# Performance work log

Hardware: AMD Instinct MI355X
Metric: run time of the kernel (lower is better)

Reference implementation:

```python
import jax, jax.numpy as jnp
import numpy as np

B, N, IN_DIM, SLOT_DIM, NUM_SLOTS, NUM_ITERS = 64, 4096, 256, 256, 8, 3
LN_EPS = 1e-5


def _ln(x, g, b):
    m = jnp.mean(x, axis=-1, keepdims=True)
    v = jnp.mean(jnp.square(x - m), axis=-1, keepdims=True)
    return (x - m) * jax.lax.rsqrt(v + LN_EPS) * g + b


def setup_inputs() -> dict:
    key = jax.random.key(0)
    ks = jax.random.split(key, 16)
    D, I = SLOT_DIM, IN_DIM
    s = 0.02
    return {
        "inputs": jax.random.normal(ks[0], (B, N, I), jnp.float32),
        "slots_noise": jax.random.normal(ks[1], (B, NUM_SLOTS, D), jnp.float32),
        "slots_mu": jax.random.normal(ks[2], (1, 1, D), jnp.float32),
        "slots_log_sigma": jnp.zeros((1, 1, D), jnp.float32),
        "ln_in_g": jnp.ones((I,), jnp.float32), "ln_in_b": jnp.zeros((I,), jnp.float32),
        "ln_s_g": jnp.ones((D,), jnp.float32), "ln_s_b": jnp.zeros((D,), jnp.float32),
        "ln_m_g": jnp.ones((D,), jnp.float32), "ln_m_b": jnp.zeros((D,), jnp.float32),
        "Wq": jax.random.normal(ks[3], (D, D), jnp.float32) * s,
        "Wk": jax.random.normal(ks[4], (I, D), jnp.float32) * s,
        "Wv": jax.random.normal(ks[5], (I, D), jnp.float32) * s,
        "gru_w_ih": jax.random.normal(ks[6], (3 * D, D), jnp.float32) * s,
        "gru_w_hh": jax.random.normal(ks[7], (3 * D, D), jnp.float32) * s,
        "gru_b_ih": jnp.zeros((3 * D,), jnp.float32),
        "gru_b_hh": jnp.zeros((3 * D,), jnp.float32),
        "mlp_w1": jax.random.normal(ks[8], (D, 4 * D), jnp.float32) * s,
        "mlp_b1": jnp.zeros((4 * D,), jnp.float32),
        "mlp_w2": jax.random.normal(ks[9], (4 * D, D), jnp.float32) * s,
        "mlp_b2": jnp.zeros((D,), jnp.float32),
    }


def reference(inputs, slots_noise, slots_mu, slots_log_sigma, ln_in_g, ln_in_b,
              ln_s_g, ln_s_b, ln_m_g, ln_m_b, Wq, Wk, Wv,
              gru_w_ih, gru_w_hh, gru_b_ih, gru_b_hh,
              mlp_w1, mlp_b1, mlp_w2, mlp_b2):
    D = SLOT_DIM
    # slot init: mu + sigma * noise
    slots = slots_mu + jnp.exp(slots_log_sigma) * slots_noise  # [B, S, D]
    x = _ln(inputs, ln_in_g, ln_in_b)                          # [B, N, I]
    k = x @ Wk                                                 # [B, N, D]
    v = x @ Wv                                                 # [B, N, D]
    scale = 1.0 / jnp.sqrt(jnp.float32(D))
    attn = None
    for _ in range(NUM_ITERS):
        slots_prev = slots
        s_n = _ln(slots, ln_s_g, ln_s_b)
        q = s_n @ Wq                                           # [B, S, D]
        logits = jnp.einsum('bnd,bmd->bnm', k, q) * scale      # [B, N, S]
        attn = jax.nn.softmax(logits, axis=-1)                 # softmax over slots
        attn_nrm = attn / (jnp.sum(attn, axis=1, keepdims=True) + 1e-8)
        updates = jnp.einsum('bnm,bnd->bmd', attn_nrm, v)      # [B, S, D]
        # GRUCell (PyTorch semantics)
        gi = updates @ gru_w_ih.T + gru_b_ih                   # [B, S, 3D]
        gh = slots_prev @ gru_w_hh.T + gru_b_hh
        gi_r, gi_z, gi_n = jnp.split(gi, 3, axis=-1)
        gh_r, gh_z, gh_n = jnp.split(gh, 3, axis=-1)
        r = jax.nn.sigmoid(gi_r + gh_r)
        z = jax.nn.sigmoid(gi_z + gh_z)
        n = jnp.tanh(gi_n + r * gh_n)
        slots = (1.0 - z) * n + z * slots_prev
        # residual MLP
        h = jax.nn.relu(_ln(slots, ln_m_g, ln_m_b) @ mlp_w1 + mlp_b1)
        slots = slots + h @ mlp_w2 + mlp_b2
    return slots, jnp.transpose(attn, (0, 2, 1))
```

## Files before the change

### kernel.cpp

```cpp
#include <hip/hip_runtime.h>


typedef unsigned short u16;
typedef __attribute__((ext_vector_type(8))) short bf16x8;
typedef __attribute__((ext_vector_type(4))) float f32x4;

#define MFMA16(a, b, c) __builtin_amdgcn_mfma_f32_16x16x32_bf16((a), (b), (c), 0, 0, 0)

__device__ __forceinline__ u16 f2bf(float f) {
  union { float f; unsigned u; } v; v.f = f;
  unsigned r = (v.u + 0x7fffu + ((v.u >> 16) & 1u)) >> 16;
  return (u16)r;
}
__device__ __forceinline__ float sigm(float x) { return 1.f / (1.f + __expf(-x)); }
__device__ __forceinline__ float tanh_f(float x) { return 1.f - 2.f / (1.f + __expf(2.f * x)); }

__global__ __launch_bounds__(256) void prep_kernel(
    const float* __restrict__ Wq, const float* __restrict__ Wk, const float* __restrict__ Wv,
    const float* __restrict__ wih, const float* __restrict__ whh,
    const float* __restrict__ w1, const float* __restrict__ w2,
    u16* __restrict__ wkB, u16* __restrict__ wqT, u16* __restrict__ wvT,
    u16* __restrict__ wihB, u16* __restrict__ whhB, u16* __restrict__ w1T, u16* __restrict__ w2T) {
  int gid = blockIdx.x * 256 + threadIdx.x;
  int stride = gridDim.x * 256;
  for (int i = gid; i < 65536; i += stride) wkB[i] = f2bf(Wk[i]);
  for (int i = gid; i < 65536; i += stride) { int d = i >> 8, e = i & 255; wqT[i] = f2bf(Wq[e * 256 + d]); }
  for (int i = gid; i < 65536; i += stride) { int d = i >> 8, ii = i & 255; wvT[i] = f2bf(Wv[ii * 256 + d]); }
  for (int i = gid; i < 196608; i += stride) wihB[i] = f2bf(wih[i]);
  for (int i = gid; i < 196608; i += stride) whhB[i] = f2bf(whh[i]);
  for (int i = gid; i < 262144; i += stride) { int j = i >> 8, e = i & 255; w1T[i] = f2bf(w1[e * 1024 + j]); }
  for (int i = gid; i < 262144; i += stride) { int d = i >> 10, j = i & 1023; w2T[i] = f2bf(w2[j * 256 + d]); }
}

__device__ __forceinline__ void ln_row16(const float (*src)[264], u16 (*dst)[264],
                                         const float* __restrict__ g, const float* __restrict__ bb,
                                         int wave, int lane) {
  int row = wave;
  if (row < 8) {
    float4 v = *reinterpret_cast<const float4*>(&src[row][lane * 4]);
    float s = v.x + v.y + v.z + v.w;
    float sq = v.x * v.x + v.y * v.y + v.z * v.z + v.w * v.w;
#pragma unroll
    for (int m = 1; m < 64; m <<= 1) { s += __shfl_xor(s, m); sq += __shfl_xor(sq, m); }
    float mu = s * (1.f / 256.f);
    float var = sq * (1.f / 256.f) - mu * mu;
    float rstd = rsqrtf(fmaxf(var, 0.f) + 1e-5f);
    float4 gg = *reinterpret_cast<const float4*>(&g[lane * 4]);
    float4 bv = *reinterpret_cast<const float4*>(&bb[lane * 4]);
    unsigned lo = (unsigned)f2bf((v.x - mu) * rstd * gg.x + bv.x) |
                  ((unsigned)f2bf((v.y - mu) * rstd * gg.y + bv.y) << 16);
    unsigned hi = (unsigned)f2bf((v.z - mu) * rstd * gg.z + bv.z) |
                  ((unsigned)f2bf((v.w - mu) * rstd * gg.w + bv.w) << 16);
    *reinterpret_cast<uint2*>(&dst[row][lane * 4]) = make_uint2(lo, hi);
  } else if (row < 16) {
    *reinterpret_cast<uint2*>(&dst[row][lane * 4]) = make_uint2(0, 0);
  }
}

__global__ __launch_bounds__(1024, 4) void slot_kernel(
    float* __restrict__ slots, u16* __restrict__ qg, float* __restrict__ cd,
    const float* __restrict__ wsY, const float* __restrict__ wsS,
    const u16* __restrict__ wvT, const u16* __restrict__ wihB, const u16* __restrict__ whhB,
    const u16* __restrict__ w1T, const u16* __restrict__ w2T, const u16* __restrict__ wqT,
    const u16* __restrict__ wkB,
    const float* __restrict__ bih, const float* __restrict__ bhh,
    const float* __restrict__ b1v, const float* __restrict__ b2v,
    const float* __restrict__ g_in, const float* __restrict__ b_in,
    const float* __restrict__ g_s, const float* __restrict__ b_s,
    const float* __restrict__ g_m, const float* __restrict__ b_m,
    const float* __restrict__ s_mu, const float* __restrict__ s_ls,
    const float* __restrict__ noise,
    float* __restrict__ d_out, int do_update) {
  __shared__ alignas(16) char pool[58368];
  u16 (*h_lds)[1032] = reinterpret_cast<u16(*)[1032]>(pool);
  u16 (*u_lds)[264] = reinterpret_cast<u16(*)[264]>(pool);
  u16 (*uv_lds)[264] = reinterpret_cast<u16(*)[264]>(pool + 8448);
  u16 (*sb_lds)[264] = reinterpret_cast<u16(*)[264]>(pool + 16896);
  u16 (*m_lds)[264] = reinterpret_cast<u16(*)[264]>(pool + 33024);
  float (*ns_lds)[264] = reinterpret_cast<float(*)[264]>(pool + 41472);
  u16 (*q_lds)[264] = reinterpret_cast<u16(*)[264]>(pool + 41472);
  __shared__ float sS0[16], sS1[16], sInv[16];
  __shared__ float redq[16][4][4][2];

  const int b = blockIdx.x;
  const int tid = threadIdx.x;
  const int lane = tid & 63, wave = tid >> 6;
  const int quad = lane >> 4, col = lane & 15;
  const int i256 = tid & 255, s4 = tid >> 8;
  const f32x4 vzero = {0.f, 0.f, 0.f, 0.f};

  if (do_update) {
    if (tid < 16) {
      float S0 = 0.f, S1 = 0.f;
      if (tid < 8) {
        for (int c = 0; c < 8; c++) {
          S0 += wsS[((b * 8 + c) * 8 + tid) * 2 + 0];
          S1 += wsS[((b * 8 + c) * 8 + tid) * 2 + 1];
        }
      }
      sS0[tid] = S0; sS1[tid] = S1; sInv[tid] = 1.f / (S0 + 1e-8f);
    }
#pragma unroll
    for (int r = 0; r < 4; r++) {
      int s = s4 + r * 4;
      sb_lds[s][i256] = (s < 8) ? f2bf(slots[(size_t)(b * 8 + s) * 256 + i256]) : (u16)0;
    }
    __syncthreads();
    {
      float gv = g_in[i256], bv = b_in[i256];
#pragma unroll
      for (int r = 0; r < 4; r++) {
        int s = s4 + r * 4;
        if (s < 8) {
          float y = 0.f;
#pragma unroll
          for (int c = 0; c < 8; c++) y += wsY[((size_t)((b * 8 + c) * 8 + s)) * 256 + i256];
          u_lds[s][i256] = f2bf((gv * (y - sS1[s]) + bv * sS0[s]) * sInv[s]);
        } else {
          u_lds[s][i256] = 0;
        }
      }
    }
    __syncthreads();
    {
      bf16x8 af[8];
#pragma unroll
      for (int k = 0; k < 8; k++)
        af[k] = *reinterpret_cast<const bf16x8*>(&u_lds[col][k * 32 + quad * 8]);
      int ct = wave;
      f32x4 acc = vzero;
#pragma unroll
      for (int k = 0; k < 8; k++) {
        bf16x8 bf = *reinterpret_cast<const bf16x8*>(wvT + (size_t)(ct * 16 + col) * 256 + k * 32 + quad * 8);
        acc = MFMA16(af[k], bf, acc);
      }
#pragma unroll
      for (int r = 0; r < 4; r++) {
        int s = quad * 4 + r;
        uv_lds[s][ct * 16 + col] = (s < 8) ? f2bf(acc[r]) : (u16)0;
      }
    }
    __syncthreads();
    {
      bf16x8 afu[8], afs[8];
#pragma unroll
      for (int k = 0; k < 8; k++) {
        afu[k] = *reinterpret_cast<const bf16x8*>(&uv_lds[col][k * 32 + quad * 8]);
        afs[k] = *reinterpret_cast<const bf16x8*>(&sb_lds[col][k * 32 + quad * 8]);
      }
      int d = wave * 16 + col;
      f32x4 a_ir = vzero, a_iz = vzero, a_in = vzero, a_hr = vzero, a_hz = vzero, a_hn = vzero;
#pragma unroll
      for (int k = 0; k < 8; k++) {
        int ko = k * 32 + quad * 8;
        a_ir = MFMA16(afu[k], *reinterpret_cast<const bf16x8*>(wihB + (size_t)(d)*256 + ko), a_ir);
        a_iz = MFMA16(afu[k], *reinterpret_cast<const bf16x8*>(wihB + (size_t)(256 + d) * 256 + ko), a_iz);
        a_in = MFMA16(afu[k], *reinterpret_cast<const bf16x8*>(wihB + (size_t)(512 + d) * 256 + ko), a_in);
        a_hr = MFMA16(afs[k], *reinterpret_cast<const bf16x8*>(whhB + (size_t)(d)*256 + ko), a_hr);
        a_hz = MFMA16(afs[k], *reinterpret_cast<const bf16x8*>(whhB + (size_t)(256 + d) * 256 + ko), a_hz);
        a_hn = MFMA16(afs[k], *reinterpret_cast<const bf16x8*>(whhB + (size_t)(512 + d) * 256 + ko), a_hn);
      }
      float bihr = bih[d], bihz = bih[256 + d], bihn = bih[512 + d];
      float bhhr = bhh[d], bhhz = bhh[256 + d], bhhn = bhh[512 + d];
#pragma unroll
      for (int r = 0; r < 4; r++) {
        int s = quad * 4 + r;
        float rg = sigm(a_ir[r] + bihr + a_hr[r] + bhhr);
        float zg = sigm(a_iz[r] + bihz + a_hz[r] + bhhz);
        float ng = tanh_f(a_in[r] + bihn + rg * (a_hn[r] + bhhn));
        float prev = (s < 8) ? slots[(size_t)(b * 8 + s) * 256 + d] : 0.f;
        float ns = (1.f - zg) * ng + zg * prev;
        ns_lds[s][d] = (s < 8) ? ns : 0.f;
      }
    }
    __syncthreads();
    ln_row16(ns_lds, m_lds, g_m, b_m, wave, lane);
    __syncthreads();
    {
      bf16x8 af[8];
#pragma unroll
      for (int k = 0; k < 8; k++)
        af[k] = *reinterpret_cast<const bf16x8*>(&m_lds[col][k * 32 + quad * 8]);
      for (int cc = 0; cc < 4; cc++) {
        int ct = wave * 4 + cc;
        f32x4 acc = vzero;
#pragma unroll
        for (int k = 0; k < 8; k++) {
          bf16x8 bf = *reinterpret_cast<const bf16x8*>(w1T + (size_t)(ct * 16 + col) * 256 + k * 32 + quad * 8);
          acc = MFMA16(af[k], bf, acc);
        }
        float bb = b1v[ct * 16 + col];
#pragma unroll
        for (int r = 0; r < 4; r++) {
          int s = quad * 4 + r;
          float h = fmaxf(acc[r] + bb, 0.f);
          h_lds[s][ct * 16 + col] = (s < 8) ? f2bf(h) : (u16)0;
        }
      }
    }
    __syncthreads();
    {
      int ct = wave;
      f32x4 acc = vzero;
      for (int k = 0; k < 32; k++) {
        bf16x8 af = *reinterpret_cast<const bf16x8*>(&h_lds[col][k * 32 + quad * 8]);
        bf16x8 bf = *reinterpret_cast<const bf16x8*>(w2T + (size_t)(ct * 16 + col) * 1024 + k * 32 + quad * 8);
        acc = MFMA16(af, bf, acc);
      }
      int d = ct * 16 + col;
      float bb = b2v[d];
#pragma unroll
      for (int r = 0; r < 4; r++) {
        int s = quad * 4 + r;
        if (s < 8) {
          float fin = ns_lds[s][d] + acc[r] + bb;
          slots[(size_t)(b * 8 + s) * 256 + d] = fin;
          d_out[(size_t)(b * 8 + s) * 256 + d] = fin;
          ns_lds[s][d] = fin;
        }
      }
    }
    __syncthreads();
  } else {
#pragma unroll
    for (int r = 0; r < 4; r++) {
      int s = s4 + r * 4;
      float v = 0.f;
      if (s < 8) {
        v = s_mu[i256] + __expf(s_ls[i256]) * noise[(size_t)(b * 8 + s) * 256 + i256];
        slots[(size_t)(b * 8 + s) * 256 + i256] = v;
      }
      ns_lds[s][i256] = v;
    }
    __syncthreads();
  }

  ln_row16(ns_lds, m_lds, g_s, b_s, wave, lane);
  __syncthreads();
  {
    bf16x8 af[8];
#pragma unroll
    for (int k = 0; k < 8; k++)
      af[k] = *reinterpret_cast<const bf16x8*>(&m_lds[col][k * 32 + quad * 8]);
    int ct = wave;
    f32x4 acc = vzero;
#pragma unroll
    for (int k = 0; k < 8; k++) {
      bf16x8 bf = *reinterpret_cast<const bf16x8*>(wqT + (size_t)(ct * 16 + col) * 256 + k * 32 + quad * 8);
      acc = MFMA16(af[k], bf, acc);
    }
#pragma unroll
    for (int r = 0; r < 4; r++) {
      int s = quad * 4 + r;
      q_lds[s][ct * 16 + col] = (s < 8) ? f2bf(acc[r]) : (u16)0;
    }
  }
  __syncthreads();
  {
    bf16x8 af[8];
#pragma unroll
    for (int k = 0; k < 8; k++)
      af[k] = *reinterpret_cast<const bf16x8*>(&q_lds[col][k * 32 + quad * 8]);
    float cacc[4] = {0.f, 0.f, 0.f, 0.f}, dacc[4] = {0.f, 0.f, 0.f, 0.f};
    int ct = wave;
    f32x4 acc = vzero;
#pragma unroll
    for (int k = 0; k < 8; k++) {
      bf16x8 bf = *reinterpret_cast<const bf16x8*>(wkB + (size_t)(ct * 16 + col) * 256 + k * 32 + quad * 8);
      acc = MFMA16(af[k], bf, acc);
    }
    int i = ct * 16 + col;
    float gi_ = g_in[i] * 0.0625f, bi_ = b_in[i] * 0.0625f;
#pragma unroll
    for (int r = 0; r < 4; r++) {
      int s = quad * 4 + r;
      float qkv = acc[r];
      float qgv = (s < 8) ? gi_ * qkv : 0.f;
      qg[(size_t)(b * 16 + s) * 256 + i] = f2bf(qgv);
      cacc[r] -= qgv;
      dacc[r] += (s < 8) ? bi_ * qkv : 0.f;
    }
#pragma unroll
    for (int r = 0; r < 4; r++) {
#pragma unroll
      for (int m = 1; m < 16; m <<= 1) {
        cacc[r] += __shfl_xor(cacc[r], m);
        dacc[r] += __shfl_xor(dacc[r], m);
      }
    }
    if (col == 0) {
#pragma unroll
      for (int r = 0; r < 4; r++) {
        redq[wave][quad][r][0] = cacc[r];
        redq[wave][quad][r][1] = dacc[r];
      }
    }
    __syncthreads();
    if (tid < 16) {
      int qd = tid >> 2, r = tid & 3;
      float c = 0.f, dd = 0.f;
      for (int w = 0; w < 16; w++) { c += redq[w][qd][r][0]; dd += redq[w][qd][r][1]; }
      cd[(b * 16 + tid) * 2 + 0] = c;
      cd[(b * 16 + tid) * 2 + 1] = dd;
    }
  }
}

__global__ __launch_bounds__(512, 4) void attn_kernel(
    const float* __restrict__ x, const u16* __restrict__ qg, const float* __restrict__ cd,
    float* __restrict__ out, float* __restrict__ wsY, float* __restrict__ wsS) {
  __shared__ alignas(16) u16 x_lds[64][264];
  __shared__ alignas(16) u16 a2t[16][72];
  __shared__ float2 stats_lds[64];
  __shared__ float2 red2[4][8];

  const int chunk = blockIdx.x, b = blockIdx.y;
  const int tid = threadIdx.x;
  const int lane = tid & 63, wave = tid >> 6;
  const int quad = lane >> 4, col = lane & 15;

  for (int idx = tid; idx < 288; idx += 512)
    reinterpret_cast<unsigned*>(&a2t[8][0])[idx] = 0;

  bf16x8 bfrag[8];
#pragma unroll
  for (int k = 0; k < 8; k++)
    bfrag[k] = *reinterpret_cast<const bf16x8*>(qg + (size_t)(b * 16 + col) * 256 + k * 32 + quad * 8);
  const float2 cdv = *reinterpret_cast<const float2*>(cd + (b * 16 + col) * 2);

  f32x4 Yacc[2];
  Yacc[0] = {0.f, 0.f, 0.f, 0.f};
  Yacc[1] = {0.f, 0.f, 0.f, 0.f};
  float s0a = 0.f, s1a = 0.f;
  float* out_attn = out + 131072;

  for (int g = 0; g < 8; g++) {
    const int nb = chunk * 512 + g * 64;
    float4 vreg[8];
#pragma unroll
    for (int p = 0; p < 8; p++)
      vreg[p] = *reinterpret_cast<const float4*>(x + (size_t)(b * 4096 + nb + wave * 8 + p) * 256 + lane * 4);
#pragma unroll
    for (int p = 0; p < 8; p++) {
      int row = wave * 8 + p;
      float4 v = vreg[p];
      float s = v.x + v.y + v.z + v.w;
      float sq = v.x * v.x + v.y * v.y + v.z * v.z + v.w * v.w;
#pragma unroll
      for (int m = 1; m < 64; m <<= 1) { s += __shfl_xor(s, m); sq += __shfl_xor(sq, m); }
      float mu = s * (1.f / 256.f);
      float var = sq * (1.f / 256.f) - mu * mu;
      float rstd = rsqrtf(fmaxf(var, 0.f) + 1e-5f);
      if (lane == 0) stats_lds[row] = make_float2(rstd, rstd * mu);
      unsigned lo = (unsigned)f2bf(v.x) | ((unsigned)f2bf(v.y) << 16);
      unsigned hi = (unsigned)f2bf(v.z) | ((unsigned)f2bf(v.w) << 16);
      *reinterpret_cast<uint2*>(&x_lds[row][lane * 4]) = make_uint2(lo, hi);
    }
    __syncthreads();
    if (wave < 4) {
      const int rowbase = wave * 16;
      f32x4 acc = {0.f, 0.f, 0.f, 0.f};
#pragma unroll
      for (int k = 0; k < 8; k++) {
        bf16x8 af = *reinterpret_cast<const bf16x8*>(&x_lds[rowbase + col][k * 32 + quad * 8]);
        acc = MFMA16(af, bfrag[k], acc);
      }
      float at[4], rmx[4], rmy[4];
#pragma unroll
      for (int r = 0; r < 4; r++) {
        float2 rm = stats_lds[rowbase + quad * 4 + r];
        rmx[r] = rm.x; rmy[r] = rm.y;
        float lg = rm.x * acc[r] + rm.y * cdv.x + cdv.y;
        float mx = lg;
        mx = fmaxf(mx, __shfl_xor(mx, 1));
        mx = fmaxf(mx, __shfl_xor(mx, 2));
        mx = fmaxf(mx, __shfl_xor(mx, 4));
        float e = __expf(lg - mx);
        float sm = e;
        sm += __shfl_xor(sm, 1); sm += __shfl_xor(sm, 2); sm += __shfl_xor(sm, 4);
        at[r] = e / sm;
      }
      if (col < 8) {
#pragma unroll
        for (int r = 0; r < 4; r++) {
          int n_loc = rowbase + quad * 4 + r;
          out_attn[(size_t)(b * 8 + col) * 4096 + nb + n_loc] = at[r];
          a2t[col][n_loc] = f2bf(at[r] * rmx[r]);
          s0a += at[r];
          s1a += at[r] * rmy[r];
        }
      }
    }
    __syncthreads();
    {
      bf16x8 af0 = *reinterpret_cast<const bf16x8*>(&a2t[col][quad * 8]);
      bf16x8 af1 = *reinterpret_cast<const bf16x8*>(&a2t[col][32 + quad * 8]);
#pragma unroll
      for (int cc = 0; cc < 2; cc++) {
        int ib = (wave * 2 + cc) * 16 + col;
        union { short s[8]; bf16x8 v; } b0, b1;
#pragma unroll
        for (int j = 0; j < 8; j++) {
          b0.s[j] = (short)x_lds[quad * 8 + j][ib];
          b1.s[j] = (short)x_lds[32 + quad * 8 + j][ib];
        }
        Yacc[cc] = MFMA16(af0, b0.v, Yacc[cc]);
        Yacc[cc] = MFMA16(af1, b1.v, Yacc[cc]);
      }
    }
    __syncthreads();
  }
  if (quad < 2) {
#pragma unroll
    for (int cc = 0; cc < 2; cc++) {
      int i = (wave * 2 + cc) * 16 + col;
#pragma unroll
      for (int r = 0; r < 4; r++) {
        int s = quad * 4 + r;
        wsY[(size_t)((b * 8 + chunk) * 8 + s) * 256 + i] = Yacc[cc][r];
      }
    }
  }
  s0a += __shfl_xor(s0a, 16); s0a += __shfl_xor(s0a, 32);
  s1a += __shfl_xor(s1a, 16); s1a += __shfl_xor(s1a, 32);
  if (wave < 4 && lane < 8) red2[wave][lane] = make_float2(s0a, s1a);
  __syncthreads();
  if (tid < 8) {
    float S0 = 0.f, S1 = 0.f;
#pragma unroll
    for (int w = 0; w < 4; w++) { S0 += red2[w][tid].x; S1 += red2[w][tid].y; }
    wsS[((b * 8 + chunk) * 8 + tid) * 2 + 0] = S0;
    wsS[((b * 8 + chunk) * 8 + tid) * 2 + 1] = S1;
  }
}

extern "C" void kernel_launch(void* const* d_in, const int* in_sizes, int n_in,
                              void* d_out, int out_size, void* d_ws, size_t ws_size,
                              hipStream_t stream) {
  const float* inputs = (const float*)d_in[0];
  const float* noise = (const float*)d_in[1];
  const float* s_mu = (const float*)d_in[2];
  const float* s_ls = (const float*)d_in[3];
  const float* g_in = (const float*)d_in[4];
  const float* b_in = (const float*)d_in[5];
  const float* g_s = (const float*)d_in[6];
  const float* b_s = (const float*)d_in[7];
  const float* g_m = (const float*)d_in[8];
  const float* b_m = (const float*)d_in[9];
  const float* Wq = (const float*)d_in[10];
  const float* Wk = (const float*)d_in[11];
  const float* Wv = (const float*)d_in[12];
  const float* wih = (const float*)d_in[13];
  const float* whh = (const float*)d_in[14];
  const float* bih = (const float*)d_in[15];
  const float* bhh = (const float*)d_in[16];
  const float* w1 = (const float*)d_in[17];
  const float* b1v = (const float*)d_in[18];
  const float* w2 = (const float*)d_in[19];
  const float* b2v = (const float*)d_in[20];
  float* out = (float*)d_out;

  size_t o = 0;
  auto take = [&](size_t bytes) {
    void* p = (char*)d_ws + o;
    o += (bytes + 255) & ~(size_t)255;
    return p;
  };
  float* slots = (float*)take((size_t)64 * 8 * 256 * 4);
  u16* qg = (u16*)take((size_t)64 * 16 * 256 * 2);
  float* cd = (float*)take((size_t)64 * 16 * 2 * 4);
  float* wsY = (float*)take((size_t)64 * 8 * 8 * 256 * 4);
  float* wsS = (float*)take((size_t)64 * 8 * 8 * 2 * 4);
  u16* wkB = (u16*)take((size_t)65536 * 2);
  u16* wqT = (u16*)take((size_t)65536 * 2);
  u16* wvT = (u16*)take((size_t)65536 * 2);
  u16* wihB = (u16*)take((size_t)196608 * 2);
  u16* whhB = (u16*)take((size_t)196608 * 2);
  u16* w1T = (u16*)take((size_t)262144 * 2);
  u16* w2T = (u16*)take((size_t)262144 * 2);

  prep_kernel<<<256, 256, 0, stream>>>(Wq, Wk, Wv, wih, whh, w1, w2,
                                       wkB, wqT, wvT, wihB, whhB, w1T, w2T);
  slot_kernel<<<64, 1024, 0, stream>>>(slots, qg, cd, wsY, wsS,
                                       wvT, wihB, whhB, w1T, w2T, wqT, wkB,
                                       bih, bhh, b1v, b2v,
                                       g_in, b_in, g_s, b_s, g_m, b_m,
                                       s_mu, s_ls, noise, out, 0);
  for (int it = 0; it < 3; it++) {
    attn_kernel<<<dim3(8, 64), 512, 0, stream>>>(inputs, qg, cd, out, wsY, wsS);
    slot_kernel<<<64, 1024, 0, stream>>>(slots, qg, cd, wsY, wsS,
                                         wvT, wihB, whhB, w1T, w2T, wqT, wkB,
                                         bih, bhh, b1v, b2v,
                                         g_in, b_in, g_s, b_s, g_m, b_m,
                                         s_mu, s_ls, noise, out, 1);
  }
}
```

Baseline: 773.1 us.

## Cache bf16 inputs and LN stats across iterations, prefetch next tile, tile prep transposes

The first attention pass now writes the bf16-converted inputs and per-row LayerNorm statistics to a workspace. Later passes read that half-size data instead of re-reading the fp32 inputs and recomputing the statistics. Each attention block also register-prefetches the next 64-row tile while computing on the current one, which removes one barrier per loop. The weight-prep kernel switches to LDS-tiled transposes and vectorized conversion. In exchange, pass 0 does extra global writes (about 128 MB of bf16 data), and more registers are held live for the prefetch buffers.

```diff
diff --git a/kernel.cpp b/kernel.cpp
--- a/kernel.cpp
+++ b/kernel.cpp
@@ -21,15 +21,43 @@
     const float* __restrict__ w1, const float* __restrict__ w2,
     u16* __restrict__ wkB, u16* __restrict__ wqT, u16* __restrict__ wvT,
     u16* __restrict__ wihB, u16* __restrict__ whhB, u16* __restrict__ w1T, u16* __restrict__ w2T) {
-  int gid = blockIdx.x * 256 + threadIdx.x;
-  int stride = gridDim.x * 256;
-  for (int i = gid; i < 65536; i += stride) wkB[i] = f2bf(Wk[i]);
-  for (int i = gid; i < 65536; i += stride) { int d = i >> 8, e = i & 255; wqT[i] = f2bf(Wq[e * 256 + d]); }
-  for (int i = gid; i < 65536; i += stride) { int d = i >> 8, ii = i & 255; wvT[i] = f2bf(Wv[ii * 256 + d]); }
-  for (int i = gid; i < 196608; i += stride) wihB[i] = f2bf(wih[i]);
-  for (int i = gid; i < 196608; i += stride) whhB[i] = f2bf(whh[i]);
-  for (int i = gid; i < 262144; i += stride) { int j = i >> 8, e = i & 255; w1T[i] = f2bf(w1[e * 1024 + j]); }
-  for (int i = gid; i < 262144; i += stride) { int d = i >> 10, j = i & 1023; w2T[i] = f2bf(w2[j * 256 + d]); }
+  const int bid = blockIdx.x;
+  const int tid = threadIdx.x;
+  if (bid < 160) {
+    __shared__ float tile[64][65];
+    const float* src; u16* dst; int R, C, t;
+    if (bid < 16)      { src = Wq; dst = wqT; R = 256;  C = 256;  t = bid; }
+    else if (bid < 32) { src = Wv; dst = wvT; R = 256;  C = 256;  t = bid - 16; }
+    else if (bid < 96) { src = w1; dst = w1T; R = 1024; C = 256;  t = bid - 32; }
+    else               { src = w2; dst = w2T; R = 256;  C = 1024; t = bid - 96; }
+    const int tilesJ = C >> 6;
+    const int i0 = (t / tilesJ) * 64, j0 = (t % tilesJ) * 64;
+    const int c = tid & 63, r0 = tid >> 6;
+#pragma unroll
+    for (int rr = 0; rr < 16; rr++) {
+      int row = rr * 4 + r0;
+      tile[row][c] = src[(size_t)(j0 + row) * R + i0 + c];
+    }
+    __syncthreads();
+#pragma unroll
+    for (int rr = 0; rr < 16; rr++) {
+      int row = rr * 4 + r0;
+      dst[(size_t)(i0 + row) * C + j0 + c] = f2bf(tile[c][row]);
+    }
+  } else {
+    int gid = (bid - 160) * 256 + tid;
+    for (int i4 = gid; i4 < 114688; i4 += 64 * 256) {
+      int i = i4 * 4;
+      const float* s; u16* d; int off;
+      if (i < 65536) { s = Wk; d = wkB; off = i; }
+      else if (i < 262144) { s = wih; d = wihB; off = i - 65536; }
+      else { s = whh; d = whhB; off = i - 262144; }
+      float4 v = *reinterpret_cast<const float4*>(s + off);
+      unsigned lo = (unsigned)f2bf(v.x) | ((unsigned)f2bf(v.y) << 16);
+      unsigned hi = (unsigned)f2bf(v.z) | ((unsigned)f2bf(v.w) << 16);
+      *reinterpret_cast<uint2*>(d + off) = make_uint2(lo, hi);
+    }
+  }
 }
 
 __device__ __forceinline__ void ln_row16(const float (*src)[264], u16 (*dst)[264],
@@ -306,8 +334,10 @@
   }
 }
 
+template <int PASS>
 __global__ __launch_bounds__(512, 4) void attn_kernel(
-    const float* __restrict__ x, const u16* __restrict__ qg, const float* __restrict__ cd,
+    const float* __restrict__ x, u16* __restrict__ xb, float2* __restrict__ stats2,
+    const u16* __restrict__ qg, const float* __restrict__ cd,
     float* __restrict__ out, float* __restrict__ wsY, float* __restrict__ wsS) {
   __shared__ alignas(16) u16 x_lds[64][264];
   __shared__ alignas(16) u16 a2t[16][72];
@@ -334,29 +364,70 @@
   float s0a = 0.f, s1a = 0.f;
   float* out_attn = out + 131072;
 
+  float4 pf0[8];
+  uint2 pf1[8];
+  float2 pfs;
+  {
+    const int nb0 = chunk * 512;
+    if (PASS == 0) {
+#pragma unroll
+      for (int p = 0; p < 8; p++)
+        pf0[p] = *reinterpret_cast<const float4*>(x + (size_t)(b * 4096 + nb0 + wave * 8 + p) * 256 + lane * 4);
+    } else {
+#pragma unroll
+      for (int p = 0; p < 8; p++)
+        pf1[p] = *reinterpret_cast<const uint2*>(xb + (size_t)(b * 4096 + nb0 + wave * 8 + p) * 256 + lane * 4);
+      if (tid < 64) pfs = stats2[(size_t)b * 4096 + nb0 + tid];
+    }
+  }
+
   for (int g = 0; g < 8; g++) {
     const int nb = chunk * 512 + g * 64;
-    float4 vreg[8];
-#pragma unroll
-    for (int p = 0; p < 8; p++)
-      vreg[p] = *reinterpret_cast<const float4*>(x + (size_t)(b * 4096 + nb + wave * 8 + p) * 256 + lane * 4);
-#pragma unroll
-    for (int p = 0; p < 8; p++) {
-      int row = wave * 8 + p;
-      float4 v = vreg[p];
-      float s = v.x + v.y + v.z + v.w;
-      float sq = v.x * v.x + v.y * v.y + v.z * v.z + v.w * v.w;
-#pragma unroll
-      for (int m = 1; m < 64; m <<= 1) { s += __shfl_xor(s, m); sq += __shfl_xor(sq, m); }
-      float mu = s * (1.f / 256.f);
-      float var = sq * (1.f / 256.f) - mu * mu;
-      float rstd = rsqrtf(fmaxf(var, 0.f) + 1e-5f);
-      if (lane == 0) stats_lds[row] = make_float2(rstd, rstd * mu);
-      unsigned lo = (unsigned)f2bf(v.x) | ((unsigned)f2bf(v.y) << 16);
-      unsigned hi = (unsigned)f2bf(v.z) | ((unsigned)f2bf(v.w) << 16);
-      *reinterpret_cast<uint2*>(&x_lds[row][lane * 4]) = make_uint2(lo, hi);
-    }
-    __syncthreads();
+    __syncthreads();
+    if (PASS == 0) {
+#pragma unroll
+      for (int p = 0; p < 8; p++) {
+        int row = wave * 8 + p;
+        float4 v = pf0[p];
+        float s = v.x + v.y + v.z + v.w;
+        float sq = v.x * v.x + v.y * v.y + v.z * v.z + v.w * v.w;
+#pragma unroll
+        for (int m = 1; m < 64; m <<= 1) { s += __shfl_xor(s, m); sq += __shfl_xor(sq, m); }
+        float mu = s * (1.f / 256.f);
+        float var = sq * (1.f / 256.f) - mu * mu;
+        float rstd = rsqrtf(fmaxf(var, 0.f) + 1e-5f);
+        float2 st = make_float2(rstd, rstd * mu);
+        if (lane == 0) {
+          stats_lds[row] = st;
+          stats2[(size_t)b * 4096 + nb + row] = st;
+        }
+        unsigned lo = (unsigned)f2bf(v.x) | ((unsigned)f2bf(v.y) << 16);
+        unsigned hi = (unsigned)f2bf(v.z) | ((unsigned)f2bf(v.w) << 16);
+        *reinterpret_cast<uint2*>(&x_lds[row][lane * 4]) = make_uint2(lo, hi);
+        *reinterpret_cast<uint2*>(xb + (size_t)(b * 4096 + nb + row) * 256 + lane * 4) = make_uint2(lo, hi);
+      }
+    } else {
+#pragma unroll
+      for (int p = 0; p < 8; p++) {
+        int row = wave * 8 + p;
+        *reinterpret_cast<uint2*>(&x_lds[row][lane * 4]) = pf1[p];
+      }
+      if (tid < 64) stats_lds[tid] = pfs;
+    }
+    __syncthreads();
+    if (g < 7) {
+      const int nbn = nb + 64;
+      if (PASS == 0) {
+#pragma unroll
+        for (int p = 0; p < 8; p++)
+          pf0[p] = *reinterpret_cast<const float4*>(x + (size_t)(b * 4096 + nbn + wave * 8 + p) * 256 + lane * 4);
+      } else {
+#pragma unroll
+        for (int p = 0; p < 8; p++)
+          pf1[p] = *reinterpret_cast<const uint2*>(xb + (size_t)(b * 4096 + nbn + wave * 8 + p) * 256 + lane * 4);
+        if (tid < 64) pfs = stats2[(size_t)b * 4096 + nbn + tid];
+      }
+    }
     if (wave < 4) {
       const int rowbase = wave * 16;
       f32x4 acc = {0.f, 0.f, 0.f, 0.f};
@@ -408,7 +479,6 @@
         Yacc[cc] = MFMA16(af1, b1.v, Yacc[cc]);
       }
     }
-    __syncthreads();
   }
   if (quad < 2) {
 #pragma unroll
@@ -478,8 +548,10 @@
   u16* whhB = (u16*)take((size_t)196608 * 2);
   u16* w1T = (u16*)take((size_t)262144 * 2);
   u16* w2T = (u16*)take((size_t)262144 * 2);
-
-  prep_kernel<<<256, 256, 0, stream>>>(Wq, Wk, Wv, wih, whh, w1, w2,
+  u16* xb = (u16*)take((size_t)64 * 4096 * 256 * 2);
+  float2* stats2 = (float2*)take((size_t)64 * 4096 * 8);
+
+  prep_kernel<<<224, 256, 0, stream>>>(Wq, Wk, Wv, wih, whh, w1, w2,
                                        wkB, wqT, wvT, wihB, whhB, w1T, w2T);
   slot_kernel<<<64, 1024, 0, stream>>>(slots, qg, cd, wsY, wsS,
                                        wvT, wihB, whhB, w1T, w2T, wqT, wkB,
@@ -487,7 +559,10 @@
                                        g_in, b_in, g_s, b_s, g_m, b_m,
                                        s_mu, s_ls, noise, out, 0);
   for (int it = 0; it < 3; it++) {
-    attn_kernel<<<dim3(8, 64), 512, 0, stream>>>(inputs, qg, cd, out, wsY, wsS);
+    if (it == 0)
+      attn_kernel<0><<<dim3(8, 64), 512, 0, stream>>>(inputs, xb, stats2, qg, cd, out, wsY, wsS);
+    else
+      attn_kernel<1><<<dim3(8, 64), 512, 0, stream>>>(inputs, xb, stats2, qg, cd, out, wsY, wsS);
     slot_kernel<<<64, 1024, 0, stream>>>(slots, qg, cd, wsY, wsS,
                                          wvT, wihB, whhB, w1T, w2T, wqT, wkB,
                                          bih, bhh, b1v, b2v,
```

After: 701.9 us. -9.2%, faster.
